# Kernel optimization log

Hardware: AMD Instinct MI355X
Metric: run time of the kernel (lower is better)

## Reference

```python
import jax, jax.numpy as jnp
import numpy as np

DIM = 1024
NUM_HEADS = 16
HEAD_DIM = DIM // NUM_HEADS
ROPE_THETA = 10000.0
SCALE = HEAD_DIM ** -0.5


def _apply_rope(x, cos, sin):
    # x: [B, H, S, head_dim]; cos/sin: [S, head_dim//2] (broadcast over B, H)
    x_even = x[..., 0::2]
    x_odd = x[..., 1::2]
    rot_even = x_even * cos - x_odd * sin
    rot_odd = x_even * sin + x_odd * cos
    # interleave back: stack on last axis then flatten, matching torch .stack(-1).flatten(-2)
    return jnp.stack([rot_even, rot_odd], axis=-1).reshape(x.shape)


def setup_inputs() -> dict:
    key = jax.random.key(0)
    k0, k1, k2 = jax.random.split(key, 3)
    B, S = 2, 2048
    x = jax.random.normal(k0, (B, S, DIM), dtype=jnp.float32)
    # small_init: std = sqrt(2 / (5*dim))
    qkv_w = jax.random.normal(k1, (3 * DIM, DIM), dtype=jnp.float32) * (2.0 / (5 * DIM)) ** 0.5
    qkv_b = jnp.zeros((3 * DIM,), dtype=jnp.float32)
    # wang_init: std = 2 / num_blocks / sqrt(dim) scaled
    out_w = jax.random.normal(k2, (DIM, DIM), dtype=jnp.float32) * (2.0 / DIM) ** 0.5 / 2.0
    out_b = jnp.zeros((DIM,), dtype=jnp.float32)
    return {"x": x, "qkv_w": qkv_w, "qkv_b": qkv_b, "out_w": out_w, "out_b": out_b, "window_size": 512}


def reference(x, qkv_w, qkv_b, out_w, out_b, window_size):
    B, S, D = x.shape
    qkv = x @ qkv_w.T + qkv_b                          # [B, S, 3D]
    qkv = qkv.reshape(B, S, 3, NUM_HEADS, HEAD_DIM).transpose(2, 0, 3, 1, 4)
    q, k, v = qkv[0], qkv[1], qkv[2]                   # each [B, H, S, hd]

    pos = jnp.arange(S, dtype=jnp.float32)
    inv_freq = 1.0 / (ROPE_THETA ** (jnp.arange(0, HEAD_DIM, 2, dtype=jnp.float32) / HEAD_DIM))
    freqs = pos[:, None] * inv_freq                    # [S, hd//2]
    cos, sin = jnp.cos(freqs), jnp.sin(freqs)
    q = _apply_rope(q, cos, sin)
    k = _apply_rope(k, cos, sin)

    scores = jnp.einsum('bhqd,bhkd->bhqk', q, k) * SCALE
    i = jnp.arange(S)
    mask = (i[:, None] >= i[None, :]) & ((i[:, None] - i[None, :]) < window_size)  # causal sliding window
    scores = jnp.where(mask, scores, -jnp.inf)
    attn = jax.nn.softmax(scores, axis=-1)
    out = jnp.einsum('bhqk,bhkd->bhqd', attn, v)       # [B, H, S, hd]
    out = out.transpose(0, 2, 1, 3).reshape(B, S, D)
    return out @ out_w.T + out_b
```

## Files before the change

kernel.cpp:

```cpp
#include <hip/hip_runtime.h>
#include <hip/hip_bf16.h>
#include <cstdint>
#include <cstddef>

using bf16x8 = __attribute__((ext_vector_type(8))) short;
using f32x4  = __attribute__((ext_vector_type(4))) float;

#define MFMA16(a, b, c) __builtin_amdgcn_mfma_f32_16x16x32_bf16((a), (b), (c), 0, 0, 0)

__device__ __forceinline__ unsigned short f2bf(float f) {
    unsigned int u = __float_as_uint(f);
    u += 0x7fffu + ((u >> 16) & 1u);
    return (unsigned short)(u >> 16);
}
__device__ __forceinline__ uint32_t pack2bf(float a, float b) {
    __hip_bfloat162 h = __float22bfloat162_rn(float2{a, b});
    return *(uint32_t*)&h;
}
__device__ __forceinline__ float bf2f(short x) {
    return __uint_as_float(((uint32_t)(unsigned short)x) << 16);
}

__device__ __forceinline__ void gload_lds16(const void* g, void* l) {
    __builtin_amdgcn_global_load_lds(
        (const __attribute__((address_space(1))) void*)g,
        (__attribute__((address_space(3))) void*)l, 16, 0, 0);
}

#define S_LEN 2048
#define NHEAD 16
#define HDIM  64
#define DIM   1024
#define WIN   512
#define MROWS 4096

__global__ void prep(float* __restrict__ cosT, float* __restrict__ sinT,
                     const float* __restrict__ x, unsigned short* __restrict__ xb,
                     const float* __restrict__ qw, unsigned short* __restrict__ qwb,
                     const float* __restrict__ ow, unsigned short* __restrict__ owb) {
    int t = blockIdx.x * 256 + threadIdx.x;
    if (t < 65536) {
        int s = t >> 5, f = t & 31;
        float invf = powf(10000.0f, -(float)f / 32.0f);
        float ang = (float)s * invf;
        cosT[t] = cosf(ang);
        sinT[t] = sinf(ang);
        return;
    }
    int u = t - 65536;
    const float* src;
    unsigned short* dst;
    int i;
    if (u < 1048576)        { src = x;  dst = xb;  i = u * 4; }
    else if (u < 1835008)   { src = qw; dst = qwb; i = (u - 1048576) * 4; }
    else                    { src = ow; dst = owb; i = (u - 1835008) * 4; }
    float4 v = *(const float4*)(src + i);
    ushort4 o;
    o.x = f2bf(v.x); o.y = f2bf(v.y); o.z = f2bf(v.z); o.w = f2bf(v.w);
    *(ushort4*)(dst + i) = o;
}

__global__ __launch_bounds__(256) void gemm_qkv_fused(
        const unsigned short* __restrict__ A,
        const unsigned short* __restrict__ Bw,
        const float* __restrict__ bias,
        const float* __restrict__ cosT, const float* __restrict__ sinT,
        unsigned short* __restrict__ qbuf,
        unsigned short* __restrict__ kbuf,
        unsigned short* __restrict__ vtb) {
    __shared__ __align__(16) char smem_raw[34816];
    const int tid = threadIdx.x;
    const int lane = tid & 63, w = tid >> 6;
    const int wr = w >> 1, wc = w & 1, lm = lane & 15, lg = lane >> 4;
    const int bx = blockIdx.x, by = blockIdx.y;
    const int row0 = by * 128, col0 = bx * 128;
    const int plane = bx >> 3;
    const int h0 = (bx & 7) * 2;
    const int b = by >> 4, s_base = (by & 15) * 128;

    f32x4 acc[4][4];
#pragma unroll
    for (int m = 0; m < 4; ++m)
#pragma unroll
        for (int n = 0; n < 4; ++n) acc[m][n] = (f32x4){0.f, 0.f, 0.f, 0.f};

    short* As = (short*)smem_raw;
    short* Bs = (short*)(smem_raw + 16384);

    for (int kt = 0; kt < 16; ++kt) {
#pragma unroll
        for (int i = 0; i < 4; ++i) {
            int c = tid + 256 * i;
            int r = c >> 3, gs = (c & 7) ^ (r & 7);
            gload_lds16((const char*)A  + (size_t)(row0 + r) * 2048 + (size_t)kt * 128 + gs * 16, As + c * 8);
            gload_lds16((const char*)Bw + (size_t)(col0 + r) * 2048 + (size_t)kt * 128 + gs * 16, Bs + c * 8);
        }
        __syncthreads();
        bf16x8 af0[4], af1[4], bf0[4], bf1[4];
#pragma unroll
        for (int m = 0; m < 4; ++m) {
            int rl = wr * 64 + m * 16 + lm, rb = rl & 7;
            af0[m] = *(const bf16x8*)&As[rl * 64 + ((lg ^ rb) << 3)];
            af1[m] = *(const bf16x8*)&As[rl * 64 + (((lg + 4) ^ rb) << 3)];
        }
#pragma unroll
        for (int n = 0; n < 4; ++n) {
            int rl = wc * 64 + n * 16 + lm, rb = rl & 7;
            bf0[n] = *(const bf16x8*)&Bs[rl * 64 + ((lg ^ rb) << 3)];
            bf1[n] = *(const bf16x8*)&Bs[rl * 64 + (((lg + 4) ^ rb) << 3)];
        }
#pragma unroll
        for (int m = 0; m < 4; ++m)
#pragma unroll
            for (int n = 0; n < 4; ++n) {
                acc[m][n] = MFMA16(af0[m], bf0[n], acc[m][n]);
                acc[m][n] = MFMA16(af1[m], bf1[n], acc[m][n]);
            }
        __syncthreads();
    }

    unsigned short (*tile)[136] = (unsigned short(*)[136])smem_raw;
    const int lane8 = tid & 7, idx = tid >> 3;

    if (plane < 2) {
#pragma unroll
        for (int m = 0; m < 4; ++m)
#pragma unroll
            for (int n = 0; n < 4; ++n) {
                int colL = wc * 64 + n * 16 + lm;
                float bv = bias[col0 + colL];
#pragma unroll
                for (int r = 0; r < 4; ++r)
                    tile[wr * 64 + m * 16 + lg * 4 + r][colL] = f2bf(acc[m][n][r] + bv);
            }
    } else {
#pragma unroll
        for (int m = 0; m < 4; ++m)
#pragma unroll
            for (int n = 0; n < 4; ++n) {
                int colL = wc * 64 + n * 16 + lm;
                float bv = bias[col0 + colL];
                uint2 pk;
                pk.x = pack2bf(acc[m][n][0] + bv, acc[m][n][1] + bv);
                pk.y = pack2bf(acc[m][n][2] + bv, acc[m][n][3] + bv);
                *(uint2*)&tile[colL][wr * 64 + m * 16 + lg * 4] = pk;
            }
    }
    __syncthreads();

    if (plane < 2) {
        unsigned short* dstp = (plane == 0) ? qbuf : kbuf;
        const float qsc = (plane == 0) ? 0.125f : 1.0f;
        int d0 = lane8 * 8;
#pragma unroll
        for (int j = 0; j < 4; ++j) {
            int srow = idx + 32 * j;
            int s = s_base + srow;
            float4 c4 = *(const float4*)&cosT[s * 32 + (d0 >> 1)];
            float4 s4 = *(const float4*)&sinT[s * 32 + (d0 >> 1)];
#pragma unroll
            for (int hh = 0; hh < 2; ++hh) {
                bf16x8 v = *(const bf16x8*)&tile[srow][hh * 64 + d0];
                float e0 = bf2f(v[0]), o0 = bf2f(v[1]);
                float e1 = bf2f(v[2]), o1 = bf2f(v[3]);
                float e2 = bf2f(v[4]), o2 = bf2f(v[5]);
                float e3 = bf2f(v[6]), o3 = bf2f(v[7]);
                uint4 pk;
                pk.x = pack2bf((e0 * c4.x - o0 * s4.x) * qsc, (e0 * s4.x + o0 * c4.x) * qsc);
                pk.y = pack2bf((e1 * c4.y - o1 * s4.y) * qsc, (e1 * s4.y + o1 * c4.y) * qsc);
                pk.z = pack2bf((e2 * c4.z - o2 * s4.z) * qsc, (e2 * s4.z + o2 * c4.z) * qsc);
                pk.w = pack2bf((e3 * c4.w - o3 * s4.w) * qsc, (e3 * s4.w + o3 * c4.w) * qsc);
                int h = h0 + hh;
                *(uint4*)&dstp[(((size_t)(b * NHEAD + h)) * S_LEN + s) * 64 + d0] = pk;
            }
        }
    } else {
#pragma unroll
        for (int rr = 0; rr < 4; ++rr) {
            int hd = rr * 32 + idx;
            int hh = hd >> 6, d = hd & 63, h = h0 + hh;
#pragma unroll
            for (int j = 0; j < 2; ++j) {
                int s0 = lane8 * 8 + j * 64;
                bf16x8 v = *(const bf16x8*)&tile[hd][s0];
                *(bf16x8*)&vtb[((size_t)(b * NHEAD + h) * 64 + d) * S_LEN +
                               s_base + s0] = v;
            }
        }
    }
}

__global__ __launch_bounds__(256) void gemm_out(const unsigned short* __restrict__ A,
                                                const unsigned short* __restrict__ Bw,
                                                const float* __restrict__ bias,
                                                float* __restrict__ Cout) {
    __shared__ __align__(16) char smem_raw[24576];
    const int tid = threadIdx.x;
    const int lane = tid & 63, w = tid >> 6;
    const int wr = w >> 1, wc = w & 1, lm = lane & 15, lg = lane >> 4;
    const int row0 = blockIdx.y * 128, col0 = blockIdx.x * 64;

    f32x4 acc[4][2];
#pragma unroll
    for (int m = 0; m < 4; ++m)
#pragma unroll
        for (int n = 0; n < 2; ++n) acc[m][n] = (f32x4){0.f, 0.f, 0.f, 0.f};

    short* As = (short*)smem_raw;
    short* Bs = (short*)(smem_raw + 16384);

    for (int kt = 0; kt < 16; ++kt) {
#pragma unroll
        for (int i = 0; i < 4; ++i) {
            int c = tid + 256 * i;
            int r = c >> 3, gs = (c & 7) ^ (r & 7);
            gload_lds16((const char*)A + (size_t)(row0 + r) * 2048 + (size_t)kt * 128 + gs * 16, As + c * 8);
        }
#pragma unroll
        for (int i = 0; i < 2; ++i) {
            int c = tid + 256 * i;
            int r = c >> 3, gs = (c & 7) ^ (r & 7);
            gload_lds16((const char*)Bw + (size_t)(col0 + r) * 2048 + (size_t)kt * 128 + gs * 16, Bs + c * 8);
        }
        __syncthreads();
        bf16x8 af0[4], af1[4], bf0[2], bf1[2];
#pragma unroll
        for (int m = 0; m < 4; ++m) {
            int rl = wr * 64 + m * 16 + lm, rb = rl & 7;
            af0[m] = *(const bf16x8*)&As[rl * 64 + ((lg ^ rb) << 3)];
            af1[m] = *(const bf16x8*)&As[rl * 64 + (((lg + 4) ^ rb) << 3)];
        }
#pragma unroll
        for (int n = 0; n < 2; ++n) {
            int rl = wc * 32 + n * 16 + lm, rb = rl & 7;
            bf0[n] = *(const bf16x8*)&Bs[rl * 64 + ((lg ^ rb) << 3)];
            bf1[n] = *(const bf16x8*)&Bs[rl * 64 + (((lg + 4) ^ rb) << 3)];
        }
#pragma unroll
        for (int m = 0; m < 4; ++m)
#pragma unroll
            for (int n = 0; n < 2; ++n) {
                acc[m][n] = MFMA16(af0[m], bf0[n], acc[m][n]);
                acc[m][n] = MFMA16(af1[m], bf1[n], acc[m][n]);
            }
        __syncthreads();
    }

#pragma unroll
    for (int m = 0; m < 4; ++m) {
        int row = row0 + wr * 64 + m * 16 + lg * 4;
#pragma unroll
        for (int n = 0; n < 2; ++n) {
            int col = col0 + wc * 32 + n * 16 + lm;
            float bv = bias[col];
#pragma unroll
            for (int r = 0; r < 4; ++r)
                Cout[(size_t)(row + r) * DIM + col] = acc[m][n][r] + bv;
        }
    }
}

__global__ __launch_bounds__(256) void attn(const unsigned short* __restrict__ qb,
                                            const unsigned short* __restrict__ kb,
                                            const unsigned short* __restrict__ vt,
                                            unsigned short* __restrict__ ao) {
    const int p = blockIdx.x;
    const int L = (p & 7) * 64 + (p >> 3);
    const int qbk = L & 15, bh = L >> 4;
    const int b = bh >> 4, h = bh & 15;
    const int tid = threadIdx.x, w = tid >> 6, lane = tid & 63;
    const int lm = lane & 15, lg = lane >> 4;
    const unsigned short* Qb = qb + (size_t)bh * S_LEN * 64;
    const unsigned short* Kb = kb + (size_t)bh * S_LEN * 64;
    const unsigned short* Vt = vt + (size_t)bh * 64 * S_LEN;
    const int q0w = qbk * 128 + w * 32;

    __shared__ short Ks[2][64 * 64];
    __shared__ short Vs[2][64 * 64];
    __shared__ short Plds[4][32 * 64];
    short* Pw = Plds[w];

    bf16x8 aq[2][2];
#pragma unroll
    for (int mi = 0; mi < 2; ++mi) {
        aq[mi][0] = *(const bf16x8*)&Qb[(q0w + mi * 16 + lm) * 64 + lg * 8];
        aq[mi][1] = *(const bf16x8*)&Qb[(q0w + mi * 16 + lm) * 64 + lg * 8 + 32];
    }

    f32x4 o[2][4];
#pragma unroll
    for (int mi = 0; mi < 2; ++mi)
#pragma unroll
        for (int n = 0; n < 4; ++n) o[mi][n] = (f32x4){0.f, 0.f, 0.f, 0.f};
    float lsum0 = 0.f, lsum1 = 0.f;

    const int t0 = (qbk >= 4) ? (2 * qbk - 8) : 0;
    const int t1 = 2 * qbk + 1;

    auto stage = [&](int kt, int buf) {
#pragma unroll
        for (int i = 0; i < 2; ++i) {
            int c = tid + 256 * i;
            int r = c >> 3, g = (c & 7) ^ (r & 7);
            gload_lds16(Kb + (size_t)(kt * 64 + r) * 64 + g * 8, &Ks[buf][c * 8]);
            gload_lds16(Vt + (size_t)r * S_LEN + kt * 64 + g * 8, &Vs[buf][c * 8]);
        }
    };

    stage(t0, 0);
    __syncthreads();
    int cur = 0;
    const int sw = lm & 7;
    for (int kt = t0; kt <= t1; ++kt) {
        if (kt < t1) stage(kt + 1, cur ^ 1);
        const int kbase = kt * 64;
        f32x4 sT[2][4];
#pragma unroll
        for (int n = 0; n < 4; ++n) {
            int rl = n * 16 + lm;
            bf16x8 bk0 = *(const bf16x8*)&Ks[cur][rl * 64 + ((lg ^ sw) << 3)];
            bf16x8 bk1 = *(const bf16x8*)&Ks[cur][rl * 64 + (((lg + 4) ^ sw) << 3)];
#pragma unroll
            for (int mi = 0; mi < 2; ++mi) {
                f32x4 z = (f32x4){0.f, 0.f, 0.f, 0.f};
                z = MFMA16(bk0, aq[mi][0], z);
                sT[mi][n] = MFMA16(bk1, aq[mi][1], z);
            }
        }
#pragma unroll
        for (int mi = 0; mi < 2; ++mi) {
            const int qq = q0w + mi * 16 + lm;
#pragma unroll
            for (int n = 0; n < 4; ++n) {
                int kk0 = kbase + n * 16 + lg * 4;
#pragma unroll
                for (int r = 0; r < 4; ++r) {
                    int d = qq - (kk0 + r);
                    float pv = ((unsigned)d < (unsigned)WIN) ? __expf(sT[mi][n][r]) : 0.f;
                    sT[mi][n][r] = pv;
                    if (mi == 0) lsum0 += pv; else lsum1 += pv;
                }
                uint2 pk;
                pk.x = pack2bf(sT[mi][n][0], sT[mi][n][1]);
                pk.y = pack2bf(sT[mi][n][2], sT[mi][n][3]);
                *(uint2*)&Pw[(mi * 16 + lm) * 64 +
                             ((((2 * n + (lg >> 1)) ^ sw) << 3) + ((lg & 1) << 2))] = pk;
            }
        }
        bf16x8 ap[2][2];
#pragma unroll
        for (int mi = 0; mi < 2; ++mi) {
            ap[mi][0] = *(const bf16x8*)&Pw[(mi * 16 + lm) * 64 + ((lg ^ sw) << 3)];
            ap[mi][1] = *(const bf16x8*)&Pw[(mi * 16 + lm) * 64 + (((lg + 4) ^ sw) << 3)];
        }
#pragma unroll
        for (int n = 0; n < 4; ++n) {
            int rl = n * 16 + lm;
            bf16x8 bv0 = *(const bf16x8*)&Vs[cur][rl * 64 + ((lg ^ sw) << 3)];
            bf16x8 bv1 = *(const bf16x8*)&Vs[cur][rl * 64 + (((lg + 4) ^ sw) << 3)];
#pragma unroll
            for (int mi = 0; mi < 2; ++mi) {
                o[mi][n] = MFMA16(ap[mi][0], bv0, o[mi][n]);
                o[mi][n] = MFMA16(ap[mi][1], bv1, o[mi][n]);
            }
        }
        __syncthreads();
        cur ^= 1;
    }
    lsum0 += __shfl_xor(lsum0, 16, 64);
    lsum0 += __shfl_xor(lsum0, 32, 64);
    lsum1 += __shfl_xor(lsum1, 16, 64);
    lsum1 += __shfl_xor(lsum1, 32, 64);
    float linv0 = 1.f / lsum0, linv1 = 1.f / lsum1;
#pragma unroll
    for (int mi = 0; mi < 2; ++mi) {
        float lv = (mi == 0) ? linv0 : linv1;
#pragma unroll
        for (int r = 0; r < 4; ++r) {
            float lr = __shfl(lv, lg * 4 + r, 64);
            int row = b * S_LEN + q0w + mi * 16 + lg * 4 + r;
#pragma unroll
            for (int n = 0; n < 4; ++n) {
                int col = h * 64 + n * 16 + lm;
                ao[(size_t)row * DIM + col] = f2bf(o[mi][n][r] * lr);
            }
        }
    }
}

extern "C" void kernel_launch(void* const* d_in, const int* in_sizes, int n_in,
                              void* d_out, int out_size, void* d_ws, size_t ws_size,
                              hipStream_t stream) {
    const float* x      = (const float*)d_in[0];
    const float* qkv_w  = (const float*)d_in[1];
    const float* qkv_b  = (const float*)d_in[2];
    const float* out_w  = (const float*)d_in[3];
    const float* out_b  = (const float*)d_in[4];
    (void)in_sizes; (void)n_in; (void)out_size; (void)ws_size;

    char* ws = (char*)d_ws;
    float*          cosT = (float*)(ws + 0);
    float*          sinT = (float*)(ws + 262144);
    unsigned short* xb   = (unsigned short*)(ws + 524288);
    unsigned short* wqb  = (unsigned short*)(ws + 8912896);
    unsigned short* owb  = (unsigned short*)(ws + 15204352);
    unsigned short* qbuf = (unsigned short*)(ws + 17301504);
    unsigned short* kbuf = (unsigned short*)(ws + 25690112);
    unsigned short* vtb  = (unsigned short*)(ws + 34078720);
    unsigned short* aob  = (unsigned short*)(ws + 42467328);

    prep<<<8448, 256, 0, stream>>>(cosT, sinT, x, xb, qkv_w, wqb, out_w, owb);

    gemm_qkv_fused<<<dim3(24, 32), 256, 0, stream>>>(xb, wqb, qkv_b, cosT, sinT,
                                                     qbuf, kbuf, vtb);

    attn<<<512, 256, 0, stream>>>(qbuf, kbuf, vtb, aob);

    gemm_out<<<dim3(16, 32), 256, 0, stream>>>(aob, owb, out_b, (float*)d_out);
}
```

Measured before the change: 97.96 us.

## Halve attention query tile to 64 rows and read V directly from global

The attention kernel now assigns 64 query rows per block (16 per wave) instead of 128, doubling the grid to 1024 blocks and shrinking per-wave register state. V tiles are no longer staged through LDS; each wave loads its V fragments straight from global memory, and only K is double-buffered. MFMA sections are wrapped in s_setprio raises. This trades fewer wasted key tiles per block and higher occupancy for more redundant K/V reads across blocks and uncoalesced, unpipelined global V loads.

```diff
diff --git a/kernel.cpp b/kernel.cpp
--- a/kernel.cpp
+++ b/kernel.cpp
@@ -265,37 +265,30 @@
                                             const unsigned short* __restrict__ vt,
                                             unsigned short* __restrict__ ao) {
     const int p = blockIdx.x;
-    const int L = (p & 7) * 64 + (p >> 3);
-    const int qbk = L & 15, bh = L >> 4;
+    const int L = (p & 7) * 128 + (p >> 3);
+    const int qblk = L & 31, bh = L >> 5;
     const int b = bh >> 4, h = bh & 15;
     const int tid = threadIdx.x, w = tid >> 6, lane = tid & 63;
     const int lm = lane & 15, lg = lane >> 4;
     const unsigned short* Qb = qb + (size_t)bh * S_LEN * 64;
     const unsigned short* Kb = kb + (size_t)bh * S_LEN * 64;
     const unsigned short* Vt = vt + (size_t)bh * 64 * S_LEN;
-    const int q0w = qbk * 128 + w * 32;
+    const int q0 = qblk * 64 + w * 16;
 
     __shared__ short Ks[2][64 * 64];
-    __shared__ short Vs[2][64 * 64];
-    __shared__ short Plds[4][32 * 64];
+    __shared__ short Plds[4][16 * 64];
     short* Pw = Plds[w];
 
-    bf16x8 aq[2][2];
-#pragma unroll
-    for (int mi = 0; mi < 2; ++mi) {
-        aq[mi][0] = *(const bf16x8*)&Qb[(q0w + mi * 16 + lm) * 64 + lg * 8];
-        aq[mi][1] = *(const bf16x8*)&Qb[(q0w + mi * 16 + lm) * 64 + lg * 8 + 32];
-    }
-
-    f32x4 o[2][4];
-#pragma unroll
-    for (int mi = 0; mi < 2; ++mi)
-#pragma unroll
-        for (int n = 0; n < 4; ++n) o[mi][n] = (f32x4){0.f, 0.f, 0.f, 0.f};
-    float lsum0 = 0.f, lsum1 = 0.f;
-
-    const int t0 = (qbk >= 4) ? (2 * qbk - 8) : 0;
-    const int t1 = 2 * qbk + 1;
+    bf16x8 aq0 = *(const bf16x8*)&Qb[(q0 + lm) * 64 + lg * 8];
+    bf16x8 aq1 = *(const bf16x8*)&Qb[(q0 + lm) * 64 + lg * 8 + 32];
+
+    f32x4 o[4];
+#pragma unroll
+    for (int n = 0; n < 4; ++n) o[n] = (f32x4){0.f, 0.f, 0.f, 0.f};
+    float lsum = 0.f;
+
+    const int qq = q0 + lm;
+    const int t0 = qblk >= 8 ? qblk - 8 : 0;
 
     auto stage = [&](int kt, int buf) {
 #pragma unroll
@@ -303,7 +296,6 @@
             int c = tid + 256 * i;
             int r = c >> 3, g = (c & 7) ^ (r & 7);
             gload_lds16(Kb + (size_t)(kt * 64 + r) * 64 + g * 8, &Ks[buf][c * 8]);
-            gload_lds16(Vt + (size_t)r * S_LEN + kt * 64 + g * 8, &Vs[buf][c * 8]);
         }
     };
 
@@ -311,81 +303,64 @@
     __syncthreads();
     int cur = 0;
     const int sw = lm & 7;
-    for (int kt = t0; kt <= t1; ++kt) {
-        if (kt < t1) stage(kt + 1, cur ^ 1);
+    for (int kt = t0; kt <= qblk; ++kt) {
+        if (kt < qblk) stage(kt + 1, cur ^ 1);
         const int kbase = kt * 64;
-        f32x4 sT[2][4];
+        f32x4 sT[4];
+        __builtin_amdgcn_s_setprio(1);
 #pragma unroll
         for (int n = 0; n < 4; ++n) {
             int rl = n * 16 + lm;
             bf16x8 bk0 = *(const bf16x8*)&Ks[cur][rl * 64 + ((lg ^ sw) << 3)];
             bf16x8 bk1 = *(const bf16x8*)&Ks[cur][rl * 64 + (((lg + 4) ^ sw) << 3)];
-#pragma unroll
-            for (int mi = 0; mi < 2; ++mi) {
-                f32x4 z = (f32x4){0.f, 0.f, 0.f, 0.f};
-                z = MFMA16(bk0, aq[mi][0], z);
-                sT[mi][n] = MFMA16(bk1, aq[mi][1], z);
-            }
-        }
-#pragma unroll
-        for (int mi = 0; mi < 2; ++mi) {
-            const int qq = q0w + mi * 16 + lm;
-#pragma unroll
-            for (int n = 0; n < 4; ++n) {
-                int kk0 = kbase + n * 16 + lg * 4;
-#pragma unroll
-                for (int r = 0; r < 4; ++r) {
-                    int d = qq - (kk0 + r);
-                    float pv = ((unsigned)d < (unsigned)WIN) ? __expf(sT[mi][n][r]) : 0.f;
-                    sT[mi][n][r] = pv;
-                    if (mi == 0) lsum0 += pv; else lsum1 += pv;
-                }
-                uint2 pk;
-                pk.x = pack2bf(sT[mi][n][0], sT[mi][n][1]);
-                pk.y = pack2bf(sT[mi][n][2], sT[mi][n][3]);
-                *(uint2*)&Pw[(mi * 16 + lm) * 64 +
-                             ((((2 * n + (lg >> 1)) ^ sw) << 3) + ((lg & 1) << 2))] = pk;
-            }
-        }
-        bf16x8 ap[2][2];
-#pragma unroll
-        for (int mi = 0; mi < 2; ++mi) {
-            ap[mi][0] = *(const bf16x8*)&Pw[(mi * 16 + lm) * 64 + ((lg ^ sw) << 3)];
-            ap[mi][1] = *(const bf16x8*)&Pw[(mi * 16 + lm) * 64 + (((lg + 4) ^ sw) << 3)];
-        }
+            f32x4 z = (f32x4){0.f, 0.f, 0.f, 0.f};
+            z = MFMA16(bk0, aq0, z);
+            sT[n] = MFMA16(bk1, aq1, z);
+        }
+        __builtin_amdgcn_s_setprio(0);
 #pragma unroll
         for (int n = 0; n < 4; ++n) {
-            int rl = n * 16 + lm;
-            bf16x8 bv0 = *(const bf16x8*)&Vs[cur][rl * 64 + ((lg ^ sw) << 3)];
-            bf16x8 bv1 = *(const bf16x8*)&Vs[cur][rl * 64 + (((lg + 4) ^ sw) << 3)];
-#pragma unroll
-            for (int mi = 0; mi < 2; ++mi) {
-                o[mi][n] = MFMA16(ap[mi][0], bv0, o[mi][n]);
-                o[mi][n] = MFMA16(ap[mi][1], bv1, o[mi][n]);
-            }
-        }
+            int kk0 = kbase + n * 16 + lg * 4;
+#pragma unroll
+            for (int r = 0; r < 4; ++r) {
+                int d = qq - (kk0 + r);
+                float pv = ((unsigned)d < (unsigned)WIN) ? __expf(sT[n][r]) : 0.f;
+                sT[n][r] = pv;
+                lsum += pv;
+            }
+            uint2 pk;
+            pk.x = pack2bf(sT[n][0], sT[n][1]);
+            pk.y = pack2bf(sT[n][2], sT[n][3]);
+            *(uint2*)&Pw[lm * 64 + ((((2 * n + (lg >> 1)) ^ sw) << 3) + ((lg & 1) << 2))] = pk;
+        }
+        bf16x8 ap0 = *(const bf16x8*)&Pw[lm * 64 + ((lg ^ sw) << 3)];
+        bf16x8 ap1 = *(const bf16x8*)&Pw[lm * 64 + (((lg + 4) ^ sw) << 3)];
+        __builtin_amdgcn_s_setprio(1);
+#pragma unroll
+        for (int n = 0; n < 4; ++n) {
+            bf16x8 bv0 = *(const bf16x8*)&Vt[(size_t)(n * 16 + lm) * S_LEN + kbase + lg * 8];
+            bf16x8 bv1 = *(const bf16x8*)&Vt[(size_t)(n * 16 + lm) * S_LEN + kbase + lg * 8 + 32];
+            o[n] = MFMA16(ap0, bv0, o[n]);
+            o[n] = MFMA16(ap1, bv1, o[n]);
+        }
+        __builtin_amdgcn_s_setprio(0);
         __syncthreads();
         cur ^= 1;
     }
-    lsum0 += __shfl_xor(lsum0, 16, 64);
-    lsum0 += __shfl_xor(lsum0, 32, 64);
-    lsum1 += __shfl_xor(lsum1, 16, 64);
-    lsum1 += __shfl_xor(lsum1, 32, 64);
-    float linv0 = 1.f / lsum0, linv1 = 1.f / lsum1;
-#pragma unroll
-    for (int mi = 0; mi < 2; ++mi) {
-        float lv = (mi == 0) ? linv0 : linv1;
+    lsum += __shfl_xor(lsum, 16, 64);
+    lsum += __shfl_xor(lsum, 32, 64);
+    float linv = 1.f / lsum;
+    float lrow[4];
+#pragma unroll
+    for (int r = 0; r < 4; ++r) lrow[r] = __shfl(linv, lg * 4 + r, 64);
+#pragma unroll
+    for (int n = 0; n < 4; ++n)
 #pragma unroll
         for (int r = 0; r < 4; ++r) {
-            float lr = __shfl(lv, lg * 4 + r, 64);
-            int row = b * S_LEN + q0w + mi * 16 + lg * 4 + r;
-#pragma unroll
-            for (int n = 0; n < 4; ++n) {
-                int col = h * 64 + n * 16 + lm;
-                ao[(size_t)row * DIM + col] = f2bf(o[mi][n][r] * lr);
-            }
-        }
-    }
+            int row = b * S_LEN + q0 + lg * 4 + r;
+            int col = h * 64 + n * 16 + lm;
+            ao[(size_t)row * DIM + col] = f2bf(o[n][r] * lrow[r]);
+        }
 }
 
 extern "C" void kernel_launch(void* const* d_in, const int* in_sizes, int n_in,
@@ -414,7 +389,7 @@
     gemm_qkv_fused<<<dim3(24, 32), 256, 0, stream>>>(xb, wqb, qkv_b, cosT, sinT,
                                                      qbuf, kbuf, vtb);
 
-    attn<<<512, 256, 0, stream>>>(qbuf, kbuf, vtb, aob);
+    attn<<<1024, 256, 0, stream>>>(qbuf, kbuf, vtb, aob);
 
     gemm_out<<<dim3(16, 32), 256, 0, stream>>>(aob, owb, out_b, (float*)d_out);
 }
```

Result: slower. 115.0 us (+17.4%).
